# Optimization experiments

Measured on AMD Instinct MI355X. Metric: run time of the kernel, lower is better.

## Reference

```python
import jax, jax.numpy as jnp
import numpy as np

N_NODES = 100000

def setup_inputs() -> dict:
    key = jax.random.key(0)
    k1, k2, k3, k4, k5 = jax.random.split(key, 5)
    node_emb = jax.random.normal(k1, (100000, 128), dtype=jnp.float32)
    edge_weight = jax.random.uniform(k2, (1600000,), dtype=jnp.float32)
    src = jax.random.randint(k3, (1600000,), 0, 100000, dtype=jnp.int32)
    dst = jax.random.randint(k4, (1600000,), 0, 100000, dtype=jnp.int32)
    W = jax.random.normal(k5, (128, 128), dtype=jnp.float32) * (1.0 / np.sqrt(128))
    return {"node_emb": node_emb, "edge_weight": edge_weight, "src": src, "dst": dst, "W": W}

def reference(node_emb, edge_weight, src, dst, W):
    # u_mul_e: gather source features, scale by per-edge scalar weight
    msg = node_emb[src] * edge_weight[:, None]          # [E, d]
    # sum reduce into destination nodes (scatter-add / segment-sum)
    agg = jax.ops.segment_sum(msg, dst, num_segments=N_NODES)  # [N, d]
    # linear_out (no bias): agg @ W^T (torch Linear applies x @ W.T)
    return agg @ W.T
```

## Files before the change

### kernel.cpp

```cpp
#include <hip/hip_runtime.h>
#include <cstdint>

typedef unsigned short u16;
typedef unsigned int   u32;
typedef unsigned char  u8;

#define DIM     128
#define TPITCH  136
#define BSH     9
#define BSIZE   512
#define NBK_MAX 256
#define CHUNK   8192

__device__ __forceinline__ u16 f2bf(float x) {
    u32 u = __float_as_uint(x);
    u32 r = u + 0x7FFFu + ((u >> 16) & 1u);
    return (u16)(r >> 16);
}

typedef __attribute__((ext_vector_type(8))) short bfrag;
typedef __attribute__((ext_vector_type(4))) float f32x4;
typedef __attribute__((ext_vector_type(2))) float f32x2;

__global__ __launch_bounds__(256) void k_count_transform(
    const float* __restrict__ A, const float* __restrict__ W,
    u16* __restrict__ Tb,
    const int* __restrict__ dst, int* __restrict__ cnt,
    int n, int E, int nCntBlk, int NBK)
{
    __shared__ u16 Wb[DIM * TPITCH];

    if (blockIdx.x < nCntBlk) {
        int* hist = (int*)Wb;
        for (int i = threadIdx.x; i < NBK; i += 256) hist[i] = 0;
        __syncthreads();
        const int base = blockIdx.x * CHUNK;
        const int end  = min(base + CHUNK, E);
        for (int i = base + threadIdx.x; i < end; i += 256)
            atomicAdd(&hist[dst[i] >> BSH], 1);
        __syncthreads();
        for (int b = threadIdx.x; b < NBK; b += 256)
            cnt[b * nCntBlk + blockIdx.x] = hist[b];
        return;
    }

    {
        const int j  = threadIdx.x >> 1;
        const int k0 = (threadIdx.x & 1) << 6;
        const float* wr = W + j * DIM + k0;
        u16* wo = Wb + j * TPITCH + k0;
#pragma unroll
        for (int k = 0; k < 64; k += 4) {
            float4 v = *(const float4*)(wr + k);
            ushort4 h;
            h.x = f2bf(v.x); h.y = f2bf(v.y); h.z = f2bf(v.z); h.w = f2bf(v.w);
            *(ushort4*)(wo + k) = h;
        }
    }
    __syncthreads();

    const int wave = threadIdx.x >> 6;
    const int lane = threadIdx.x & 63;
    const int quad = lane >> 4;
    const int l16  = lane & 15;

    const int r0 = (((blockIdx.x - nCntBlk) << 2) + wave) << 4;
    if (r0 >= n) return;

    const int ar = min(r0 + l16, n - 1);
    const float* arow = A + (size_t)ar * DIM;

    f32x4 acc[8];
#pragma unroll
    for (int c = 0; c < 8; ++c) acc[c] = (f32x4)(0.f);

#pragma unroll
    for (int s = 0; s < 4; ++s) {
        const int koff = (s << 5) + (quad << 3);
        const float4 f0 = *(const float4*)(arow + koff);
        const float4 f1 = *(const float4*)(arow + koff + 4);
        bfrag a;
        a[0] = (short)f2bf(f0.x); a[1] = (short)f2bf(f0.y);
        a[2] = (short)f2bf(f0.z); a[3] = (short)f2bf(f0.w);
        a[4] = (short)f2bf(f1.x); a[5] = (short)f2bf(f1.y);
        a[6] = (short)f2bf(f1.z); a[7] = (short)f2bf(f1.w);
#pragma unroll
        for (int c = 0; c < 8; ++c) {
            const int nn = (c << 4) + l16;
            const bfrag b = *(const bfrag*)(Wb + nn * TPITCH + koff);
            acc[c] = __builtin_amdgcn_mfma_f32_16x16x32_bf16(a, b, acc[c], 0, 0, 0);
        }
    }

#pragma unroll
    for (int r = 0; r < 4; ++r) {
        const int row = r0 + (quad << 2) + r;
        if (row < n) {
            u16* orow = Tb + (size_t)row * DIM + l16;
#pragma unroll
            for (int c = 0; c < 8; ++c)
                orow[c << 4] = f2bf(acc[c][r]);
        }
    }
}

__global__ __launch_bounds__(256) void k_rowsum(
    const int* __restrict__ cnt, int* __restrict__ tot, int nCntBlk)
{
    __shared__ int red[256];
    const int t = threadIdx.x;
    const int* row = cnt + blockIdx.x * nCntBlk;
    int s = 0;
    for (int i = t; i < nCntBlk; i += 256) s += row[i];
    red[t] = s; __syncthreads();
    for (int o = 128; o; o >>= 1) {
        if (t < o) red[t] += red[t + o];
        __syncthreads();
    }
    if (t == 0) tot[blockIdx.x] = red[0];
}

__global__ __launch_bounds__(256) void k_scan_buckets(
    const int* __restrict__ tot, int* __restrict__ bucketStart, int NBK, int E)
{
    __shared__ int sc[256];
    const int t = threadIdx.x;
    const int v = (t < NBK) ? tot[t] : 0;
    sc[t] = v; __syncthreads();
    for (int d = 1; d < 256; d <<= 1) {
        int u = (t >= d) ? sc[t - d] : 0;
        __syncthreads();
        sc[t] += u;
        __syncthreads();
    }
    if (t < NBK) bucketStart[t] = sc[t] - v;
    if (t == 0) bucketStart[NBK] = E;
}

__global__ __launch_bounds__(256) void k_rowscan(
    int* __restrict__ cnt, const int* __restrict__ bucketStart, int nCntBlk)
{
    __shared__ int sc[256];
    const int t = threadIdx.x;
    int* row = cnt + blockIdx.x * nCntBlk;
    const int v = (t < nCntBlk) ? row[t] : 0;
    sc[t] = v; __syncthreads();
    for (int d = 1; d < 256; d <<= 1) {
        int u = (t >= d) ? sc[t - d] : 0;
        __syncthreads();
        sc[t] += u;
        __syncthreads();
    }
    if (t < nCntBlk) row[t] = bucketStart[blockIdx.x] + sc[t] - v;
}

__global__ __launch_bounds__(512) void k_scatter(
    const int* __restrict__ src, const int* __restrict__ dst,
    const float* __restrict__ w, const int* __restrict__ cnt,
    const int* __restrict__ bucketStart,
    int2* __restrict__ es1, int E, int nCntBlk, int NBK)
{
    __shared__ int2 buf[CHUNK];
    __shared__ u8   bid[CHUNK];
    __shared__ int  gbase[NBK_MAX];
    __shared__ int  lbase[NBK_MAX];
    __shared__ int  lpos[NBK_MAX];
    __shared__ int  sc[256];

    const int blk  = blockIdx.x;
    const int base = blk * CHUNK;
    const int end  = min(base + CHUNK, E);
    const int len  = end - base;
    const int t    = threadIdx.x;

    int mylen = 0;
    if (t < NBK) {
        const int g = cnt[t * nCntBlk + blk];
        gbase[t] = g;
        const int nxt = (blk + 1 < nCntBlk) ? cnt[t * nCntBlk + blk + 1]
                                            : bucketStart[t + 1];
        mylen = nxt - g;
    }
    if (t < 256) sc[t] = (t < NBK) ? mylen : 0;
    __syncthreads();
    for (int d = 1; d < 256; d <<= 1) {
        int v = 0;
        if (t < 256 && t >= d) v = sc[t - d];
        __syncthreads();
        if (t < 256) sc[t] += v;
        __syncthreads();
    }
    if (t < NBK) {
        const int ex = sc[t] - mylen;
        lbase[t] = ex;
        lpos[t]  = ex;
    }
    __syncthreads();

    for (int i = base + t; i < end; i += 512) {
        const int d   = dst[i];
        const int bkt = d >> BSH;
        const int p   = atomicAdd(&lpos[bkt], 1);
        buf[p] = make_int2(src[i] | ((d & (BSIZE - 1)) << 20),
                           __float_as_int(w[i]));
        bid[p] = (u8)bkt;
    }
    __syncthreads();

    for (int i = t; i < len; i += 512) {
        const int bkt = bid[i];
        es1[gbase[bkt] + (i - lbase[bkt])] = buf[i];
    }
}

__global__ __launch_bounds__(512) void k_fine(
    const int2* __restrict__ es1, const int* __restrict__ bucketStart,
    int2* __restrict__ es2, int* __restrict__ off, int n, int NBK)
{
    __shared__ int c[BSIZE];
    __shared__ int cur[BSIZE];
    __shared__ int sc[BSIZE];

    const int b = blockIdx.x;
    const int s = bucketStart[b], e = bucketStart[b + 1];
    const int t = threadIdx.x;

    c[t] = 0;
    __syncthreads();
    for (int i = s + t; i < e; i += 512)
        atomicAdd(&c[es1[i].x >> 20], 1);
    __syncthreads();

    const int myc = c[t];
    sc[t] = myc; __syncthreads();
    for (int d = 1; d < 512; d <<= 1) {
        int v = (t >= d) ? sc[t - d] : 0;
        __syncthreads();
        sc[t] += v;
        __syncthreads();
    }
    const int p = s + sc[t] - myc;
    cur[t] = p;

    const int v0 = (b << BSH) + t;
    if (v0 < n) off[v0] = p;
    if (b == NBK - 1 && t == 0) off[n] = e;
    __syncthreads();

    for (int i = s + t; i < e; i += 512) {
        const int2 ev = es1[i];
        const int pp = atomicAdd(&cur[ev.x >> 20], 1);
        es2[pp] = make_int2(ev.x & 0xFFFFF, ev.y);
    }
}

__global__ __launch_bounds__(256) void gnn_aggregate(
    const u16* __restrict__ Tb, const int* __restrict__ off,
    const int2* __restrict__ es, float* __restrict__ out, int n)
{
    const int lane = threadIdx.x & 63;
    const int wv   = threadIdx.x >> 6;
    const u32* Tw  = (const u32*)Tb;
    const int ngrp = (n + 3) >> 2;

    for (int g = blockIdx.x; g < ngrp; g += gridDim.x) {
        const int v = (g << 2) + wv;
        if (v >= n) continue;

        const int b = off[v], e = off[v + 1];
        float ax0 = 0.f, ay0 = 0.f, ax1 = 0.f, ay1 = 0.f;

        int i = b;
        for (; i + 7 < e; i += 8) {
            const int2 e0 = es[i],     e1 = es[i + 1], e2 = es[i + 2], e3 = es[i + 3];
            const int2 e4 = es[i + 4], e5 = es[i + 5], e6 = es[i + 6], e7 = es[i + 7];
            const u32 t0 = Tw[(size_t)e0.x * 64 + lane];
            const u32 t1 = Tw[(size_t)e1.x * 64 + lane];
            const u32 t2 = Tw[(size_t)e2.x * 64 + lane];
            const u32 t3 = Tw[(size_t)e3.x * 64 + lane];
            const u32 t4 = Tw[(size_t)e4.x * 64 + lane];
            const u32 t5 = Tw[(size_t)e5.x * 64 + lane];
            const u32 t6 = Tw[(size_t)e6.x * 64 + lane];
            const u32 t7 = Tw[(size_t)e7.x * 64 + lane];
            const float w0 = __int_as_float(e0.y), w1 = __int_as_float(e1.y);
            const float w2 = __int_as_float(e2.y), w3 = __int_as_float(e3.y);
            const float w4 = __int_as_float(e4.y), w5 = __int_as_float(e5.y);
            const float w6 = __int_as_float(e6.y), w7 = __int_as_float(e7.y);
            ax0 += w0 * __uint_as_float(t0 << 16);
            ay0 += w0 * __uint_as_float(t0 & 0xFFFF0000u);
            ax1 += w1 * __uint_as_float(t1 << 16);
            ay1 += w1 * __uint_as_float(t1 & 0xFFFF0000u);
            ax0 += w2 * __uint_as_float(t2 << 16);
            ay0 += w2 * __uint_as_float(t2 & 0xFFFF0000u);
            ax1 += w3 * __uint_as_float(t3 << 16);
            ay1 += w3 * __uint_as_float(t3 & 0xFFFF0000u);
            ax0 += w4 * __uint_as_float(t4 << 16);
            ay0 += w4 * __uint_as_float(t4 & 0xFFFF0000u);
            ax1 += w5 * __uint_as_float(t5 << 16);
            ay1 += w5 * __uint_as_float(t5 & 0xFFFF0000u);
            ax0 += w6 * __uint_as_float(t6 << 16);
            ay0 += w6 * __uint_as_float(t6 & 0xFFFF0000u);
            ax1 += w7 * __uint_as_float(t7 << 16);
            ay1 += w7 * __uint_as_float(t7 & 0xFFFF0000u);
        }
        for (; i + 3 < e; i += 4) {
            const int2 e0 = es[i], e1 = es[i + 1], e2 = es[i + 2], e3 = es[i + 3];
            const u32 t0 = Tw[(size_t)e0.x * 64 + lane];
            const u32 t1 = Tw[(size_t)e1.x * 64 + lane];
            const u32 t2 = Tw[(size_t)e2.x * 64 + lane];
            const u32 t3 = Tw[(size_t)e3.x * 64 + lane];
            const float w0 = __int_as_float(e0.y), w1 = __int_as_float(e1.y);
            const float w2 = __int_as_float(e2.y), w3 = __int_as_float(e3.y);
            ax0 += w0 * __uint_as_float(t0 << 16);
            ay0 += w0 * __uint_as_float(t0 & 0xFFFF0000u);
            ax1 += w1 * __uint_as_float(t1 << 16);
            ay1 += w1 * __uint_as_float(t1 & 0xFFFF0000u);
            ax0 += w2 * __uint_as_float(t2 << 16);
            ay0 += w2 * __uint_as_float(t2 & 0xFFFF0000u);
            ax1 += w3 * __uint_as_float(t3 << 16);
            ay1 += w3 * __uint_as_float(t3 & 0xFFFF0000u);
        }
        for (; i < e; ++i) {
            const int2 ev = es[i];
            const u32 t = Tw[(size_t)ev.x * 64 + lane];
            const float w0 = __int_as_float(ev.y);
            ax0 += w0 * __uint_as_float(t << 16);
            ay0 += w0 * __uint_as_float(t & 0xFFFF0000u);
        }

        f32x2 r;
        r[0] = ax0 + ax1;
        r[1] = ay0 + ay1;
        __builtin_nontemporal_store(r, (f32x2*)(out + (size_t)v * DIM + 2 * lane));
    }
}

extern "C" void kernel_launch(void* const* d_in, const int* in_sizes, int n_in,
                              void* d_out, int out_size, void* d_ws, size_t ws_size,
                              hipStream_t stream)
{
    const float* node_emb = (const float*)d_in[0];
    const float* ew       = (const float*)d_in[1];
    const int*   src      = (const int*)d_in[2];
    const int*   dst      = (const int*)d_in[3];
    const float* W        = (const float*)d_in[4];
    float* out = (float*)d_out;

    const int n = in_sizes[0] / DIM;
    const int E = in_sizes[1];
    const int NBK = (n + BSIZE - 1) >> BSH;
    const int nCntBlk = (E + CHUNK - 1) / CHUNK;
    const int M = NBK * nCntBlk;

    char* ws = (char*)d_ws;
    size_t o = 0;
    u16* Tb = (u16*)(ws + o);  o += (((size_t)n * DIM * sizeof(u16)) + 255) & ~255ULL;
    int* cnt = (int*)(ws + o); o += (((size_t)M * sizeof(int)) + 255) & ~255ULL;
    int* tot = (int*)(ws + o); o += (((size_t)NBK * sizeof(int)) + 255) & ~255ULL;
    int* bucketStart = (int*)(ws + o); o += (((size_t)(NBK + 1) * sizeof(int)) + 255) & ~255ULL;
    int* off = (int*)(ws + o); o += (((size_t)(n + 1) * sizeof(int)) + 255) & ~255ULL;
    int2* es1 = (int2*)(ws + o); o += (((size_t)E * sizeof(int2)) + 255) & ~255ULL;
    int2* es2 = (int2*)(ws + o);

    const int ntiles = (n + 63) >> 6;

    k_count_transform<<<nCntBlk + ntiles, 256, 0, stream>>>(
        node_emb, W, Tb, dst, cnt, n, E, nCntBlk, NBK);

    k_rowsum<<<NBK, 256, 0, stream>>>(cnt, tot, nCntBlk);
    k_scan_buckets<<<1, 256, 0, stream>>>(tot, bucketStart, NBK, E);
    k_rowscan<<<NBK, 256, 0, stream>>>(cnt, bucketStart, nCntBlk);

    k_scatter<<<nCntBlk, 512, 0, stream>>>(src, dst, ew, cnt, bucketStart,
                                           es1, E, nCntBlk, NBK);

    k_fine<<<NBK, 512, 0, stream>>>(es1, bucketStart, es2, off, n, NBK);

    gnn_aggregate<<<2048, 256, 0, stream>>>(Tb, off, es2, out, n);
}
```

Before: 243.4 us.

## Switch aggregation to edge-balanced wave partitioning and shrink sort buckets

```diff
diff --git a/kernel.cpp b/kernel.cpp
--- a/kernel.cpp
+++ b/kernel.cpp
@@ -3,14 +3,14 @@
 
 typedef unsigned short u16;
 typedef unsigned int   u32;
-typedef unsigned char  u8;
 
 #define DIM     128
 #define TPITCH  136
-#define BSH     9
-#define BSIZE   512
-#define NBK_MAX 256
-#define CHUNK   8192
+#define BSH     8
+#define BSIZE   256
+#define NBK_MAX 512
+#define CHUNK   4096
+#define EPW     192
 
 __device__ __forceinline__ u16 f2bf(float x) {
     u32 u = __float_as_uint(x);
@@ -120,14 +120,14 @@
     if (t == 0) tot[blockIdx.x] = red[0];
 }
 
-__global__ __launch_bounds__(256) void k_scan_buckets(
+__global__ __launch_bounds__(512) void k_scan_buckets(
     const int* __restrict__ tot, int* __restrict__ bucketStart, int NBK, int E)
 {
-    __shared__ int sc[256];
+    __shared__ int sc[512];
     const int t = threadIdx.x;
     const int v = (t < NBK) ? tot[t] : 0;
     sc[t] = v; __syncthreads();
-    for (int d = 1; d < 256; d <<= 1) {
+    for (int d = 1; d < 512; d <<= 1) {
         int u = (t >= d) ? sc[t - d] : 0;
         __syncthreads();
         sc[t] += u;
@@ -137,15 +137,15 @@
     if (t == 0) bucketStart[NBK] = E;
 }
 
-__global__ __launch_bounds__(256) void k_rowscan(
+__global__ __launch_bounds__(512) void k_rowscan(
     int* __restrict__ cnt, const int* __restrict__ bucketStart, int nCntBlk)
 {
-    __shared__ int sc[256];
+    __shared__ int sc[512];
     const int t = threadIdx.x;
     int* row = cnt + blockIdx.x * nCntBlk;
     const int v = (t < nCntBlk) ? row[t] : 0;
     sc[t] = v; __syncthreads();
-    for (int d = 1; d < 256; d <<= 1) {
+    for (int d = 1; d < 512; d <<= 1) {
         int u = (t >= d) ? sc[t - d] : 0;
         __syncthreads();
         sc[t] += u;
@@ -161,11 +161,11 @@
     int2* __restrict__ es1, int E, int nCntBlk, int NBK)
 {
     __shared__ int2 buf[CHUNK];
-    __shared__ u8   bid[CHUNK];
+    __shared__ u16  bid[CHUNK];
     __shared__ int  gbase[NBK_MAX];
     __shared__ int  lbase[NBK_MAX];
     __shared__ int  lpos[NBK_MAX];
-    __shared__ int  sc[256];
+    __shared__ int  sc[512];
 
     const int blk  = blockIdx.x;
     const int base = blk * CHUNK;
@@ -181,13 +181,12 @@
                                             : bucketStart[t + 1];
         mylen = nxt - g;
     }
-    if (t < 256) sc[t] = (t < NBK) ? mylen : 0;
-    __syncthreads();
-    for (int d = 1; d < 256; d <<= 1) {
-        int v = 0;
-        if (t < 256 && t >= d) v = sc[t - d];
-        __syncthreads();
-        if (t < 256) sc[t] += v;
+    sc[t] = (t < NBK) ? mylen : 0;
+    __syncthreads();
+    for (int d = 1; d < 512; d <<= 1) {
+        int v = (t >= d) ? sc[t - d] : 0;
+        __syncthreads();
+        sc[t] += v;
         __syncthreads();
     }
     if (t < NBK) {
@@ -203,7 +202,7 @@
         const int p   = atomicAdd(&lpos[bkt], 1);
         buf[p] = make_int2(src[i] | ((d & (BSIZE - 1)) << 20),
                            __float_as_int(w[i]));
-        bid[p] = (u8)bkt;
+        bid[p] = (u16)bkt;
     }
     __syncthreads();
 
@@ -225,25 +224,28 @@
     const int s = bucketStart[b], e = bucketStart[b + 1];
     const int t = threadIdx.x;
 
-    c[t] = 0;
+    if (t < BSIZE) c[t] = 0;
     __syncthreads();
     for (int i = s + t; i < e; i += 512)
         atomicAdd(&c[es1[i].x >> 20], 1);
     __syncthreads();
 
-    const int myc = c[t];
-    sc[t] = myc; __syncthreads();
-    for (int d = 1; d < 512; d <<= 1) {
-        int v = (t >= d) ? sc[t - d] : 0;
-        __syncthreads();
-        sc[t] += v;
-        __syncthreads();
-    }
-    const int p = s + sc[t] - myc;
-    cur[t] = p;
-
-    const int v0 = (b << BSH) + t;
-    if (v0 < n) off[v0] = p;
+    int myc = 0;
+    if (t < BSIZE) { myc = c[t]; sc[t] = myc; }
+    __syncthreads();
+    for (int d = 1; d < BSIZE; d <<= 1) {
+        int v = 0;
+        if (t < BSIZE && t >= d) v = sc[t - d];
+        __syncthreads();
+        if (t < BSIZE) sc[t] += v;
+        __syncthreads();
+    }
+    if (t < BSIZE) {
+        const int p = s + sc[t] - myc;
+        cur[t] = p;
+        const int v0 = (b << BSH) + t;
+        if (v0 < n) off[v0] = p;
+    }
     if (b == NBK - 1 && t == 0) off[n] = e;
     __syncthreads();
 
@@ -256,82 +258,82 @@
 
 __global__ __launch_bounds__(256) void gnn_aggregate(
     const u16* __restrict__ Tb, const int* __restrict__ off,
-    const int2* __restrict__ es, float* __restrict__ out, int n)
+    const int2* __restrict__ es, float* __restrict__ out, int n, int E)
 {
     const int lane = threadIdx.x & 63;
-    const int wv   = threadIdx.x >> 6;
+    const int wid  = (blockIdx.x << 2) + (threadIdx.x >> 6);
+    const int base = wid * EPW;
+    if (base >= E) return;
+    const int rend = base + EPW;
     const u32* Tw  = (const u32*)Tb;
-    const int ngrp = (n + 3) >> 2;
-
-    for (int g = blockIdx.x; g < ngrp; g += gridDim.x) {
-        const int v = (g << 2) + wv;
-        if (v >= n) continue;
-
-        const int b = off[v], e = off[v + 1];
-        float ax0 = 0.f, ay0 = 0.f, ax1 = 0.f, ay1 = 0.f;
-
-        int i = b;
-        for (; i + 7 < e; i += 8) {
-            const int2 e0 = es[i],     e1 = es[i + 1], e2 = es[i + 2], e3 = es[i + 3];
-            const int2 e4 = es[i + 4], e5 = es[i + 5], e6 = es[i + 6], e7 = es[i + 7];
-            const u32 t0 = Tw[(size_t)e0.x * 64 + lane];
-            const u32 t1 = Tw[(size_t)e1.x * 64 + lane];
-            const u32 t2 = Tw[(size_t)e2.x * 64 + lane];
-            const u32 t3 = Tw[(size_t)e3.x * 64 + lane];
-            const u32 t4 = Tw[(size_t)e4.x * 64 + lane];
-            const u32 t5 = Tw[(size_t)e5.x * 64 + lane];
-            const u32 t6 = Tw[(size_t)e6.x * 64 + lane];
-            const u32 t7 = Tw[(size_t)e7.x * 64 + lane];
-            const float w0 = __int_as_float(e0.y), w1 = __int_as_float(e1.y);
-            const float w2 = __int_as_float(e2.y), w3 = __int_as_float(e3.y);
-            const float w4 = __int_as_float(e4.y), w5 = __int_as_float(e5.y);
-            const float w6 = __int_as_float(e6.y), w7 = __int_as_float(e7.y);
-            ax0 += w0 * __uint_as_float(t0 << 16);
-            ay0 += w0 * __uint_as_float(t0 & 0xFFFF0000u);
-            ax1 += w1 * __uint_as_float(t1 << 16);
-            ay1 += w1 * __uint_as_float(t1 & 0xFFFF0000u);
-            ax0 += w2 * __uint_as_float(t2 << 16);
-            ay0 += w2 * __uint_as_float(t2 & 0xFFFF0000u);
-            ax1 += w3 * __uint_as_float(t3 << 16);
-            ay1 += w3 * __uint_as_float(t3 & 0xFFFF0000u);
-            ax0 += w4 * __uint_as_float(t4 << 16);
-            ay0 += w4 * __uint_as_float(t4 & 0xFFFF0000u);
-            ax1 += w5 * __uint_as_float(t5 << 16);
-            ay1 += w5 * __uint_as_float(t5 & 0xFFFF0000u);
-            ax0 += w6 * __uint_as_float(t6 << 16);
-            ay0 += w6 * __uint_as_float(t6 & 0xFFFF0000u);
-            ax1 += w7 * __uint_as_float(t7 << 16);
-            ay1 += w7 * __uint_as_float(t7 & 0xFFFF0000u);
+
+    int lo = 0, hi = n;
+    while (lo < hi) { const int mid = (lo + hi) >> 1; if (off[mid] < base) lo = mid + 1; else hi = mid; }
+    int v = lo;
+    int v1;
+    if (rend >= E) v1 = n;
+    else {
+        int l2 = v, h2 = n;
+        while (l2 < h2) { const int mid = (l2 + h2) >> 1; if (off[mid] < rend) l2 = mid + 1; else h2 = mid; }
+        v1 = l2;
+    }
+    if (v >= v1) return;
+
+    const int sbeg = off[v];
+    const int send = off[v1];
+
+    while (v < v1 && off[v + 1] == sbeg) {
+        f32x2 z; z[0] = 0.f; z[1] = 0.f;
+        __builtin_nontemporal_store(z, (f32x2*)(out + (size_t)v * DIM + 2 * lane));
+        ++v;
+    }
+    if (v >= v1) return;
+
+    int segEnd = off[v + 1];
+    float ax0 = 0.f, ay0 = 0.f, ax1 = 0.f, ay1 = 0.f;
+    const int send1 = send - 1;
+
+    for (int i = sbeg; i < send; i += 8) {
+        const int2 e0 = es[i];
+        const int2 e1 = es[min(i + 1, send1)];
+        const int2 e2 = es[min(i + 2, send1)];
+        const int2 e3 = es[min(i + 3, send1)];
+        const int2 e4 = es[min(i + 4, send1)];
+        const int2 e5 = es[min(i + 5, send1)];
+        const int2 e6 = es[min(i + 6, send1)];
+        const int2 e7 = es[min(i + 7, send1)];
+        const u32 t0 = Tw[(size_t)e0.x * 64 + lane];
+        const u32 t1 = Tw[(size_t)e1.x * 64 + lane];
+        const u32 t2 = Tw[(size_t)e2.x * 64 + lane];
+        const u32 t3 = Tw[(size_t)e3.x * 64 + lane];
+        const u32 t4 = Tw[(size_t)e4.x * 64 + lane];
+        const u32 t5 = Tw[(size_t)e5.x * 64 + lane];
+        const u32 t6 = Tw[(size_t)e6.x * 64 + lane];
+        const u32 t7 = Tw[(size_t)e7.x * 64 + lane];
+
+#define STEP(K, EV, TV, AX, AY)                                               \
+        if (i + K < send) {                                                   \
+            const float wgt = __int_as_float(EV.y);                           \
+            AX += wgt * __uint_as_float(TV << 16);                            \
+            AY += wgt * __uint_as_float(TV & 0xFFFF0000u);                    \
+            while (i + K + 1 == segEnd) {                                     \
+                f32x2 r; r[0] = ax0 + ax1; r[1] = ay0 + ay1;                  \
+                __builtin_nontemporal_store(r,                                \
+                    (f32x2*)(out + (size_t)v * DIM + 2 * lane));              \
+                ax0 = ay0 = ax1 = ay1 = 0.f;                                  \
+                ++v;                                                          \
+                segEnd = (v < v1) ? off[v + 1] : -1;                          \
+            }                                                                 \
         }
-        for (; i + 3 < e; i += 4) {
-            const int2 e0 = es[i], e1 = es[i + 1], e2 = es[i + 2], e3 = es[i + 3];
-            const u32 t0 = Tw[(size_t)e0.x * 64 + lane];
-            const u32 t1 = Tw[(size_t)e1.x * 64 + lane];
-            const u32 t2 = Tw[(size_t)e2.x * 64 + lane];
-            const u32 t3 = Tw[(size_t)e3.x * 64 + lane];
-            const float w0 = __int_as_float(e0.y), w1 = __int_as_float(e1.y);
-            const float w2 = __int_as_float(e2.y), w3 = __int_as_float(e3.y);
-            ax0 += w0 * __uint_as_float(t0 << 16);
-            ay0 += w0 * __uint_as_float(t0 & 0xFFFF0000u);
-            ax1 += w1 * __uint_as_float(t1 << 16);
-            ay1 += w1 * __uint_as_float(t1 & 0xFFFF0000u);
-            ax0 += w2 * __uint_as_float(t2 << 16);
-            ay0 += w2 * __uint_as_float(t2 & 0xFFFF0000u);
-            ax1 += w3 * __uint_as_float(t3 << 16);
-            ay1 += w3 * __uint_as_float(t3 & 0xFFFF0000u);
-        }
-        for (; i < e; ++i) {
-            const int2 ev = es[i];
-            const u32 t = Tw[(size_t)ev.x * 64 + lane];
-            const float w0 = __int_as_float(ev.y);
-            ax0 += w0 * __uint_as_float(t << 16);
-            ay0 += w0 * __uint_as_float(t & 0xFFFF0000u);
-        }
-
-        f32x2 r;
-        r[0] = ax0 + ax1;
-        r[1] = ay0 + ay1;
-        __builtin_nontemporal_store(r, (f32x2*)(out + (size_t)v * DIM + 2 * lane));
+        STEP(0, e0, t0, ax0, ay0)
+        STEP(1, e1, t1, ax1, ay1)
+        STEP(2, e2, t2, ax0, ay0)
+        STEP(3, e3, t3, ax1, ay1)
+        STEP(4, e4, t4, ax0, ay0)
+        STEP(5, e5, t5, ax1, ay1)
+        STEP(6, e6, t6, ax0, ay0)
+        STEP(7, e7, t7, ax1, ay1)
+#undef STEP
     }
 }
 
@@ -368,13 +370,14 @@
         node_emb, W, Tb, dst, cnt, n, E, nCntBlk, NBK);
 
     k_rowsum<<<NBK, 256, 0, stream>>>(cnt, tot, nCntBlk);
-    k_scan_buckets<<<1, 256, 0, stream>>>(tot, bucketStart, NBK, E);
-    k_rowscan<<<NBK, 256, 0, stream>>>(cnt, bucketStart, nCntBlk);
+    k_scan_buckets<<<1, 512, 0, stream>>>(tot, bucketStart, NBK, E);
+    k_rowscan<<<NBK, 512, 0, stream>>>(cnt, bucketStart, nCntBlk);
 
     k_scatter<<<nCntBlk, 512, 0, stream>>>(src, dst, ew, cnt, bucketStart,
                                            es1, E, nCntBlk, NBK);
 
     k_fine<<<NBK, 512, 0, stream>>>(es1, bucketStart, es2, off, n, NBK);
 
-    gnn_aggregate<<<2048, 256, 0, stream>>>(Tb, off, es2, out, n);
-}
+    const int nw = (E + EPW - 1) / EPW;
+    gnn_aggregate<<<(nw + 3) / 4, 256, 0, stream>>>(Tb, off, es2, out, n, E);
+}
```

Result: slower. 269.3 us (+10.6%).

## Halve bucket size, double bucket count, and fuse bucket and row scans

Applied to the files above, without the earlier changes.

```diff
diff --git a/kernel.cpp b/kernel.cpp
--- a/kernel.cpp
+++ b/kernel.cpp
@@ -3,14 +3,13 @@
 
 typedef unsigned short u16;
 typedef unsigned int   u32;
-typedef unsigned char  u8;
 
 #define DIM     128
 #define TPITCH  136
-#define BSH     9
-#define BSIZE   512
-#define NBK_MAX 256
-#define CHUNK   8192
+#define BSH     8
+#define BSIZE   256
+#define NBK_MAX 512
+#define CHUNK   4096
 
 __device__ __forceinline__ u16 f2bf(float x) {
     u32 u = __float_as_uint(x);
@@ -120,38 +119,40 @@
     if (t == 0) tot[blockIdx.x] = red[0];
 }
 
-__global__ __launch_bounds__(256) void k_scan_buckets(
-    const int* __restrict__ tot, int* __restrict__ bucketStart, int NBK, int E)
-{
-    __shared__ int sc[256];
+__global__ __launch_bounds__(512) void k_scan_all(
+    const int* __restrict__ tot, int* __restrict__ bucketStart,
+    int* __restrict__ cnt, int NBK, int nCntBlk, int E)
+{
+    __shared__ int sc[512];
+    __shared__ int bs;
     const int t = threadIdx.x;
+    const int b = blockIdx.x;
+
     const int v = (t < NBK) ? tot[t] : 0;
     sc[t] = v; __syncthreads();
-    for (int d = 1; d < 256; d <<= 1) {
+    for (int d = 1; d < 512; d <<= 1) {
         int u = (t >= d) ? sc[t - d] : 0;
         __syncthreads();
         sc[t] += u;
         __syncthreads();
     }
-    if (t < NBK) bucketStart[t] = sc[t] - v;
-    if (t == 0) bucketStart[NBK] = E;
-}
-
-__global__ __launch_bounds__(256) void k_rowscan(
-    int* __restrict__ cnt, const int* __restrict__ bucketStart, int nCntBlk)
-{
-    __shared__ int sc[256];
-    const int t = threadIdx.x;
-    int* row = cnt + blockIdx.x * nCntBlk;
-    const int v = (t < nCntBlk) ? row[t] : 0;
-    sc[t] = v; __syncthreads();
-    for (int d = 1; d < 256; d <<= 1) {
+    if (t == b) bs = sc[t] - v;
+    if (b == 0) {
+        if (t < NBK) bucketStart[t] = sc[t] - v;
+        if (t == 0)  bucketStart[NBK] = E;
+    }
+    __syncthreads();
+
+    int* row = cnt + b * nCntBlk;
+    const int rv = (t < nCntBlk) ? row[t] : 0;
+    sc[t] = rv; __syncthreads();
+    for (int d = 1; d < 512; d <<= 1) {
         int u = (t >= d) ? sc[t - d] : 0;
         __syncthreads();
         sc[t] += u;
         __syncthreads();
     }
-    if (t < nCntBlk) row[t] = bucketStart[blockIdx.x] + sc[t] - v;
+    if (t < nCntBlk) row[t] = bs + sc[t] - rv;
 }
 
 __global__ __launch_bounds__(512) void k_scatter(
@@ -161,11 +162,11 @@
     int2* __restrict__ es1, int E, int nCntBlk, int NBK)
 {
     __shared__ int2 buf[CHUNK];
-    __shared__ u8   bid[CHUNK];
+    __shared__ u16  bid[CHUNK];
     __shared__ int  gbase[NBK_MAX];
     __shared__ int  lbase[NBK_MAX];
     __shared__ int  lpos[NBK_MAX];
-    __shared__ int  sc[256];
+    __shared__ int  sc[512];
 
     const int blk  = blockIdx.x;
     const int base = blk * CHUNK;
@@ -181,13 +182,12 @@
                                             : bucketStart[t + 1];
         mylen = nxt - g;
     }
-    if (t < 256) sc[t] = (t < NBK) ? mylen : 0;
-    __syncthreads();
-    for (int d = 1; d < 256; d <<= 1) {
-        int v = 0;
-        if (t < 256 && t >= d) v = sc[t - d];
-        __syncthreads();
-        if (t < 256) sc[t] += v;
+    sc[t] = (t < NBK) ? mylen : 0;
+    __syncthreads();
+    for (int d = 1; d < 512; d <<= 1) {
+        int v = (t >= d) ? sc[t - d] : 0;
+        __syncthreads();
+        sc[t] += v;
         __syncthreads();
     }
     if (t < NBK) {
@@ -203,7 +203,7 @@
         const int p   = atomicAdd(&lpos[bkt], 1);
         buf[p] = make_int2(src[i] | ((d & (BSIZE - 1)) << 20),
                            __float_as_int(w[i]));
-        bid[p] = (u8)bkt;
+        bid[p] = (u16)bkt;
     }
     __syncthreads();
 
@@ -225,25 +225,28 @@
     const int s = bucketStart[b], e = bucketStart[b + 1];
     const int t = threadIdx.x;
 
-    c[t] = 0;
+    if (t < BSIZE) c[t] = 0;
     __syncthreads();
     for (int i = s + t; i < e; i += 512)
         atomicAdd(&c[es1[i].x >> 20], 1);
     __syncthreads();
 
-    const int myc = c[t];
-    sc[t] = myc; __syncthreads();
-    for (int d = 1; d < 512; d <<= 1) {
-        int v = (t >= d) ? sc[t - d] : 0;
-        __syncthreads();
-        sc[t] += v;
-        __syncthreads();
-    }
-    const int p = s + sc[t] - myc;
-    cur[t] = p;
-
-    const int v0 = (b << BSH) + t;
-    if (v0 < n) off[v0] = p;
+    int myc = 0;
+    if (t < BSIZE) { myc = c[t]; sc[t] = myc; }
+    __syncthreads();
+    for (int d = 1; d < BSIZE; d <<= 1) {
+        int v = 0;
+        if (t < BSIZE && t >= d) v = sc[t - d];
+        __syncthreads();
+        if (t < BSIZE) sc[t] += v;
+        __syncthreads();
+    }
+    if (t < BSIZE) {
+        const int p = s + sc[t] - myc;
+        cur[t] = p;
+        const int v0 = (b << BSH) + t;
+        if (v0 < n) off[v0] = p;
+    }
     if (b == NBK - 1 && t == 0) off[n] = e;
     __syncthreads();
 
@@ -368,8 +371,7 @@
         node_emb, W, Tb, dst, cnt, n, E, nCntBlk, NBK);
 
     k_rowsum<<<NBK, 256, 0, stream>>>(cnt, tot, nCntBlk);
-    k_scan_buckets<<<1, 256, 0, stream>>>(tot, bucketStart, NBK, E);
-    k_rowscan<<<NBK, 256, 0, stream>>>(cnt, bucketStart, nCntBlk);
+    k_scan_all<<<NBK, 512, 0, stream>>>(tot, bucketStart, cnt, NBK, nCntBlk, E);
 
     k_scatter<<<nCntBlk, 512, 0, stream>>>(src, dst, ew, cnt, bucketStart,
                                            es1, E, nCntBlk, NBK);
```

After: 236.0 us. 1.03x faster.
